# Performance work log

Measured on AMD Instinct MI355X. Metric: run time of the kernel, lower is better.

## Reference

```python
import jax, jax.numpy as jnp
import numpy as np

B, S, D, H = 2, 2048, 1024, 16
EPS = 1e-7  # keras backend epsilon

def setup_inputs() -> dict:
    key = jax.random.key(0)
    ks = jax.random.split(key, 5)
    x = jax.random.normal(ks[0], (B, S, D), dtype=jnp.float32)
    # mem_mask convention: attend where mem_mask == 0 (causal here)
    i = jnp.arange(S)
    causal = (i[None, :] > i[:, None]).astype(jnp.float32)  # 1 = masked
    mem_mask = jnp.broadcast_to(causal[None, None], (B, 1, S, S))
    Wqkv = jax.random.normal(ks[1], (D, 3 * D), dtype=jnp.float32) * (D ** -0.5)
    W_out = jax.random.normal(ks[2], (D, D), dtype=jnp.float32) * (D ** -0.5)
    b_out = jnp.zeros((D,), dtype=jnp.float32)
    scale = jnp.ones((D,), dtype=jnp.float32)
    gate = jax.random.normal(ks[3], (D,), dtype=jnp.float32) * 0.02
    return {"x": x, "mem_mask": mem_mask, "Wqkv": Wqkv, "W_out": W_out,
            "b_out": b_out, "scale": scale, "gate": gate}

def reference(x, mem_mask, Wqkv, W_out, b_out, scale, gate):
    b, s, d = x.shape
    dh = d // H
    h = jnp.einsum('bsd,de->bse', x, Wqkv)
    q, k, v = jnp.split(h, 3, axis=-1)
    def split_heads(t):
        return t.reshape(b, s, H, dh).transpose(0, 2, 1, 3)  # [B,H,S,dh]
    q, k, v = split_heads(q), split_heads(k), split_heads(v)
    q = q * (dh ** -0.5)
    logits = jnp.einsum('bhqd,bhkd->bhqk', q, k)
    logits = logits * (mem_mask == 0.0).astype(logits.dtype)
    weights = jax.nn.relu(logits)
    o = jnp.einsum('bhqk,bhkd->bhqd', weights, v)
    o = o.transpose(0, 2, 1, 3).reshape(b, s, d)  # combine heads
    # Gated RMSNorm
    ms = jnp.mean(o * o, axis=-1, keepdims=True)
    o = scale * o * jax.lax.rsqrt(ms + EPS) * jax.nn.sigmoid(gate * o)
    return jnp.einsum('bsd,de->bse', o, W_out) + b_out
```

## Files before the change

### kernel.cpp

```cpp
#include <hip/hip_runtime.h>
#include <hip/hip_bf16.h>

typedef unsigned short u16;
typedef __attribute__((ext_vector_type(8))) short bf16x8;
typedef __attribute__((ext_vector_type(4))) short short4v;
typedef __attribute__((ext_vector_type(4))) float floatx4;
typedef __attribute__((ext_vector_type(2))) unsigned uint2v;

__device__ __forceinline__ float bf2f(u16 u) {
    unsigned v = ((unsigned)u) << 16;
    return __builtin_bit_cast(float, v);
}
__device__ __forceinline__ u16 f2bf(float f) {
    unsigned u = __builtin_bit_cast(unsigned, f);
    u += 0x7fffu + ((u >> 16) & 1u);
    return (u16)(u >> 16);
}

#define GLDS16(g, l)                                                             \
    __builtin_amdgcn_global_load_lds(                                            \
        (const __attribute__((address_space(1))) void*)(g),                      \
        (__attribute__((address_space(3))) void*)(l), 16, 0, 0)

__global__ __launch_bounds__(256) void cvt_bf16(const float* __restrict__ in, u16* __restrict__ out) {
    const int i = blockIdx.x * 256 + threadIdx.x;
    const floatx4 v = ((const floatx4*)in)[i];
    short4v o;
#pragma unroll
    for (int j = 0; j < 4; ++j) o[j] = (short)f2bf(v[j]);
    ((short4v*)out)[i] = o;
}

__global__ void wtrans(const float* __restrict__ in, u16* __restrict__ out, int R, int C) {
    __shared__ u16 t[32][33];
    const int c0 = blockIdx.x * 32, r0 = blockIdx.y * 32;
    const int x = threadIdx.x, y = threadIdx.y;
#pragma unroll
    for (int i = 0; i < 32; i += 8) t[y + i][x] = f2bf(in[(size_t)(r0 + y + i) * C + c0 + x]);
    __syncthreads();
#pragma unroll
    for (int i = 0; i < 32; i += 8) out[(size_t)(c0 + y + i) * R + r0 + x] = t[x][y + i];
}

__global__ void vtrans(const u16* __restrict__ h, u16* __restrict__ vt) {
    __shared__ u16 t[32][33];
    const int bh = blockIdx.z;
    const int b = bh >> 4, hd = bh & 15;
    const int s0 = blockIdx.x * 32, d0 = blockIdx.y * 32;
    const int x = threadIdx.x, y = threadIdx.y;
    const u16* in = h + (size_t)(b * 2048) * 3072 + 2048 + hd * 64;
#pragma unroll
    for (int i = 0; i < 32; i += 8) t[y + i][x] = in[(size_t)(s0 + y + i) * 3072 + d0 + x];
    __syncthreads();
    u16* o = vt + (size_t)bh * 64 * 2048;
#pragma unroll
    for (int i = 0; i < 32; i += 8) {
        const float f = bf2f(t[x][y + i]) * 0.125f;
        o[(size_t)(d0 + y + i) * 2048 + s0 + x] = (u16)(__builtin_bit_cast(unsigned, f) >> 16);
    }
}

template <int TM, bool BIAS, typename OUT>
__global__ __launch_bounds__(256) void gemm_bt(const u16* __restrict__ A, const u16* __restrict__ Bt,
                                               OUT* __restrict__ C, const float* __restrict__ bias,
                                               int M, int N, int K) {
    constexpr int MI = TM / 32;
    __shared__ u16 sA[TM * 32];
    __shared__ u16 sB[128 * 32];
    const int tid = threadIdx.x;
    const int lane = tid & 63, wave = tid >> 6;
    const int l15 = lane & 15, quad = lane >> 4;
    const int row0 = blockIdx.y * TM, col0 = blockIdx.x * 128;
    const int wm = (wave & 1) * (TM / 2), wn = (wave >> 1) * 64;
    const int c_ = (tid & 3) << 3;
    floatx4 acc[MI][4] = {};
    for (int k0 = 0; k0 < K; k0 += 32) {
#pragma unroll
        for (int it = 0; it < 2; ++it) {
            const int idx = it * 256 + tid;
            const int r = idx >> 2;
            GLDS16(Bt + (size_t)(col0 + r) * K + k0 + c_, sB + idx * 8);
        }
#pragma unroll
        for (int it = 0; it < TM / 64; ++it) {
            const int idx = it * 256 + tid;
            const int r = idx >> 2;
            GLDS16(A + (size_t)(row0 + r) * K + k0 + c_, sA + idx * 8);
        }
        __syncthreads();
        bf16x8 af[MI], bfr[4];
#pragma unroll
        for (int i = 0; i < MI; ++i) af[i] = *(const bf16x8*)(sA + (wm + i * 16 + l15) * 32 + quad * 8);
#pragma unroll
        for (int j = 0; j < 4; ++j) bfr[j] = *(const bf16x8*)(sB + (wn + j * 16 + l15) * 32 + quad * 8);
#pragma unroll
        for (int i = 0; i < MI; ++i)
#pragma unroll
            for (int j = 0; j < 4; ++j)
                acc[i][j] = __builtin_amdgcn_mfma_f32_16x16x32_bf16(af[i], bfr[j], acc[i][j], 0, 0, 0);
        __syncthreads();
    }
#pragma unroll
    for (int i = 0; i < MI; ++i) {
#pragma unroll
        for (int j = 0; j < 4; ++j) {
            const int col = col0 + wn + j * 16 + l15;
            const int row = row0 + wm + i * 16 + quad * 4;
            const float b = BIAS ? bias[col] : 0.f;
#pragma unroll
            for (int r = 0; r < 4; ++r) {
                const float v = acc[i][j][r] + b;
                if constexpr (sizeof(OUT) == 2)
                    C[(size_t)(row + r) * N + col] = (OUT)f2bf(v);
                else
                    C[(size_t)(row + r) * N + col] = (OUT)v;
            }
        }
    }
}

__device__ __forceinline__ void pack_store(floatx4 s, u16* dst, bool diag, int kgb, int qg) {
    float v0 = fmaxf(s[0], 0.f), v1 = fmaxf(s[1], 0.f);
    float v2 = fmaxf(s[2], 0.f), v3 = fmaxf(s[3], 0.f);
    if (diag) {
        if (kgb + 0 > qg) v0 = 0.f;
        if (kgb + 1 > qg) v1 = 0.f;
        if (kgb + 2 > qg) v2 = 0.f;
        if (kgb + 3 > qg) v3 = 0.f;
    }
    uint2v p;
    p.x = ((__builtin_bit_cast(unsigned, v0) + 0x8000u) >> 16) |
          ((__builtin_bit_cast(unsigned, v1) + 0x8000u) & 0xffff0000u);
    p.y = ((__builtin_bit_cast(unsigned, v2) + 0x8000u) >> 16) |
          ((__builtin_bit_cast(unsigned, v3) + 0x8000u) & 0xffff0000u);
    *(uint2v*)dst = p;
}

__global__ __launch_bounds__(256) void relu_attn(const u16* __restrict__ h, const u16* __restrict__ vt,
                                                 float* __restrict__ o) {
    __shared__ u16 sK[64 * 72];
    __shared__ u16 sV[64 * 72];
    __shared__ u16 sP[128 * 72];
    const int bid = blockIdx.x;
    const int pr = bid >> 5;
    const int bh = bid & 31;
    const int b = bh >> 4, hd = bh & 15;
    const int qtl = pr, qth = 31 - pr;
    const int tid = threadIdx.x, lane = tid & 63, wave = tid >> 6;
    const int l15 = lane & 15, quad = lane >> 4;

    bf16x8 qfl[2], qfh[2];
    {
        const u16* ql = h + (size_t)(b * 2048 + qtl * 64 + wave * 16 + l15) * 3072 + hd * 64;
        const u16* qh = h + (size_t)(b * 2048 + qth * 64 + wave * 16 + l15) * 3072 + hd * 64;
#pragma unroll
        for (int ks = 0; ks < 2; ++ks) {
            qfl[ks] = *(const bf16x8*)(ql + ks * 32 + quad * 8);
            qfh[ks] = *(const bf16x8*)(qh + ks * 32 + quad * 8);
        }
    }

    floatx4 accl[4] = {}, acch[4] = {};
    const u16* kbase = h + (size_t)(b * 2048) * 3072 + 1024 + hd * 64;
    const u16* vbase = vt + (size_t)bh * 64 * 2048;
    const int sr = tid >> 3;
    const int sc = (tid & 7) << 3;
    const int qg = wave * 16 + l15;

    for (int kc = 0; kc <= qth; ++kc) {
        const int c0 = kc * 64;
#pragma unroll
        for (int it = 0; it < 2; ++it) {
            const int r = it * 32 + sr;
            bf16x8 kv = *(const bf16x8*)(kbase + (size_t)(c0 + r) * 3072 + sc);
            bf16x8 vv = *(const bf16x8*)(vbase + (size_t)r * 2048 + c0 + sc);
            *(bf16x8*)(sK + r * 72 + sc) = kv;
            *(bf16x8*)(sV + r * 72 + sc) = vv;
        }
        __syncthreads();
        const bool lact = (kc <= qtl);
        const floatx4 z = {0.f, 0.f, 0.f, 0.f};
#pragma unroll
        for (int mt = 0; mt < 4; ++mt) {
            const bf16x8 kf0 = *(const bf16x8*)(sK + (mt * 16 + l15) * 72 + quad * 8);
            const bf16x8 kf1 = *(const bf16x8*)(sK + (mt * 16 + l15) * 72 + 32 + quad * 8);
            const int kgb = mt * 16 + quad * 4;
            floatx4 s = __builtin_amdgcn_mfma_f32_16x16x32_bf16(kf0, qfh[0], z, 0, 0, 0);
            s = __builtin_amdgcn_mfma_f32_16x16x32_bf16(kf1, qfh[1], s, 0, 0, 0);
            pack_store(s, sP + (size_t)(64 + qg) * 72 + kgb, kc == qth, kgb, qg);
            if (lact) {
                floatx4 t = __builtin_amdgcn_mfma_f32_16x16x32_bf16(kf0, qfl[0], z, 0, 0, 0);
                t = __builtin_amdgcn_mfma_f32_16x16x32_bf16(kf1, qfl[1], t, 0, 0, 0);
                pack_store(t, sP + (size_t)qg * 72 + kgb, kc == qtl, kgb, qg);
            }
        }
#pragma unroll
        for (int kb = 0; kb < 2; ++kb) {
            const bf16x8 pfh = *(const bf16x8*)(sP + (size_t)(64 + wave * 16 + l15) * 72 + kb * 32 + quad * 8);
#pragma unroll
            for (int nt = 0; nt < 4; ++nt) {
                const bf16x8 vf = *(const bf16x8*)(sV + (nt * 16 + l15) * 72 + kb * 32 + quad * 8);
                acch[nt] = __builtin_amdgcn_mfma_f32_16x16x32_bf16(pfh, vf, acch[nt], 0, 0, 0);
                if (lact) {
                    const bf16x8 pfl = *(const bf16x8*)(sP + (size_t)(wave * 16 + l15) * 72 + kb * 32 + quad * 8);
                    accl[nt] = __builtin_amdgcn_mfma_f32_16x16x32_bf16(pfl, vf, accl[nt], 0, 0, 0);
                }
            }
        }
        __syncthreads();
    }
#pragma unroll
    for (int nt = 0; nt < 4; ++nt) {
        const int col = hd * 64 + nt * 16 + l15;
        const int rl = qtl * 64 + wave * 16 + quad * 4;
        const int rh = qth * 64 + wave * 16 + quad * 4;
#pragma unroll
        for (int r = 0; r < 4; ++r) {
            o[(size_t)(b * 2048 + rl + r) * 1024 + col] = accl[nt][r];
            o[(size_t)(b * 2048 + rh + r) * 1024 + col] = acch[nt][r];
        }
    }
}

__global__ __launch_bounds__(256) void rms_gate(const float* __restrict__ o, const float* __restrict__ scale,
                                                const float* __restrict__ gate, u16* __restrict__ out) {
    const int row = blockIdx.x;
    const int tid = threadIdx.x;
    const floatx4* op = (const floatx4*)(o + (size_t)row * 1024);
    floatx4 v = op[tid];
    float ss = v[0] * v[0] + v[1] * v[1] + v[2] * v[2] + v[3] * v[3];
#pragma unroll
    for (int m = 32; m >= 1; m >>= 1) ss += __shfl_xor(ss, m, 64);
    __shared__ float red[4];
    if ((tid & 63) == 0) red[tid >> 6] = ss;
    __syncthreads();
    const float ms = (red[0] + red[1] + red[2] + red[3]) * (1.0f / 1024.0f);
    const float inv = rsqrtf(ms + 1e-7f);
    const int c = tid * 4;
#pragma unroll
    for (int j = 0; j < 4; ++j) {
        const float s = scale[c + j];
        const float g = gate[c + j];
        const float x = v[j];
        const float sig = 1.0f / (1.0f + __expf(-g * x));
        out[(size_t)row * 1024 + c + j] = f2bf(s * x * inv * sig);
    }
}

extern "C" void kernel_launch(void* const* d_in, const int* in_sizes, int n_in,
                              void* d_out, int out_size, void* d_ws, size_t ws_size,
                              hipStream_t stream) {
    const float* x     = (const float*)d_in[0];
    const float* Wqkv  = (const float*)d_in[2];
    const float* Wout  = (const float*)d_in[3];
    const float* bout  = (const float*)d_in[4];
    const float* scale = (const float*)d_in[5];
    const float* gate  = (const float*)d_in[6];
    float* out = (float*)d_out;

    char* p = (char*)d_ws;
    u16* xb    = (u16*)p; p += (size_t)4096 * 1024 * 2;
    u16* h     = (u16*)p; p += (size_t)4096 * 3072 * 2;
    u16* vt    = (u16*)p; p += (size_t)32 * 64 * 2048 * 2;
    u16* WqkvT = (u16*)p; p += (size_t)3072 * 1024 * 2;
    u16* WoutT = (u16*)p; p += (size_t)1024 * 1024 * 2;
    float* oat = (float*)p; p += (size_t)4096 * 1024 * 4;
    u16* onorm = (u16*)p; p += (size_t)4096 * 1024 * 2;

    cvt_bf16<<<4096, 256, 0, stream>>>(x, xb);
    wtrans<<<dim3(96, 32), dim3(32, 8), 0, stream>>>(Wqkv, WqkvT, 1024, 3072);
    wtrans<<<dim3(32, 32), dim3(32, 8), 0, stream>>>(Wout, WoutT, 1024, 1024);
    gemm_bt<128, false, u16><<<dim3(24, 32), 256, 0, stream>>>(xb, WqkvT, h, nullptr, 4096, 3072, 1024);
    vtrans<<<dim3(64, 2, 32), dim3(32, 8), 0, stream>>>(h, vt);
    relu_attn<<<512, 256, 0, stream>>>(h, vt, oat);
    rms_gate<<<4096, 256, 0, stream>>>(oat, scale, gate, onorm);
    gemm_bt<64, true, float><<<dim3(8, 64), 256, 0, stream>>>(onorm, WoutT, out, bout, 4096, 1024, 1024);
}
```

Baseline: 225.4 us.

## Split causal attention over key ranges with atomic accumulation for more blocks

Replaces the paired low/high query-tile scheme with a split-K style decomposition. Each block processes one query tile over a range of at most eight key chunks, launching 2560 blocks instead of 512. Partial outputs are accumulated with float atomicAdd into a buffer that the conversion kernel now zeroes. This aims to fix low occupancy and load imbalance, at the cost of atomic traffic, an extra zeroing write, and nondeterministic summation order.

```diff
diff --git a/kernel.cpp b/kernel.cpp
--- a/kernel.cpp
+++ b/kernel.cpp
@@ -22,13 +22,16 @@
         (const __attribute__((address_space(1))) void*)(g),                      \
         (__attribute__((address_space(3))) void*)(l), 16, 0, 0)
 
-__global__ __launch_bounds__(256) void cvt_bf16(const float* __restrict__ in, u16* __restrict__ out) {
+__global__ __launch_bounds__(256) void cvt_bf16(const float* __restrict__ in, u16* __restrict__ out,
+                                                float* __restrict__ oz) {
     const int i = blockIdx.x * 256 + threadIdx.x;
     const floatx4 v = ((const floatx4*)in)[i];
     short4v o;
 #pragma unroll
     for (int j = 0; j < 4; ++j) o[j] = (short)f2bf(v[j]);
     ((short4v*)out)[i] = o;
+    const floatx4 z = {0.f, 0.f, 0.f, 0.f};
+    ((floatx4*)oz)[i] = z;
 }
 
 __global__ void wtrans(const float* __restrict__ in, u16* __restrict__ out, int R, int C) {
@@ -140,34 +143,33 @@
                                                  float* __restrict__ o) {
     __shared__ u16 sK[64 * 72];
     __shared__ u16 sV[64 * 72];
-    __shared__ u16 sP[128 * 72];
+    __shared__ u16 sP[64 * 72];
     const int bid = blockIdx.x;
-    const int pr = bid >> 5;
     const int bh = bid & 31;
+    const int p = bid >> 5;
+    int s, qt;
+    if (p < 32)      { s = 0; qt = 31 - p; }
+    else if (p < 56) { s = 1; qt = 31 - (p - 32); }
+    else if (p < 72) { s = 2; qt = 31 - (p - 56); }
+    else             { s = 3; qt = 31 - (p - 72); }
     const int b = bh >> 4, hd = bh & 15;
-    const int qtl = pr, qth = 31 - pr;
     const int tid = threadIdx.x, lane = tid & 63, wave = tid >> 6;
     const int l15 = lane & 15, quad = lane >> 4;
-
-    bf16x8 qfl[2], qfh[2];
-    {
-        const u16* ql = h + (size_t)(b * 2048 + qtl * 64 + wave * 16 + l15) * 3072 + hd * 64;
-        const u16* qh = h + (size_t)(b * 2048 + qth * 64 + wave * 16 + l15) * 3072 + hd * 64;
-#pragma unroll
-        for (int ks = 0; ks < 2; ++ks) {
-            qfl[ks] = *(const bf16x8*)(ql + ks * 32 + quad * 8);
-            qfh[ks] = *(const bf16x8*)(qh + ks * 32 + quad * 8);
-        }
-    }
-
-    floatx4 accl[4] = {}, acch[4] = {};
+    const int q0 = qt * 64;
+    const int c_lo = s * 8, c_hi = min(s * 8 + 7, qt);
+
+    const u16* qrow = h + (size_t)(b * 2048 + q0 + wave * 16 + l15) * 3072 + hd * 64;
+    bf16x8 qf0 = *(const bf16x8*)(qrow + quad * 8);
+    bf16x8 qf1 = *(const bf16x8*)(qrow + 32 + quad * 8);
+
+    floatx4 acc[4] = {};
     const u16* kbase = h + (size_t)(b * 2048) * 3072 + 1024 + hd * 64;
     const u16* vbase = vt + (size_t)bh * 64 * 2048;
     const int sr = tid >> 3;
     const int sc = (tid & 7) << 3;
     const int qg = wave * 16 + l15;
 
-    for (int kc = 0; kc <= qth; ++kc) {
+    for (int kc = c_lo; kc <= c_hi; ++kc) {
         const int c0 = kc * 64;
 #pragma unroll
         for (int it = 0; it < 2; ++it) {
@@ -178,33 +180,24 @@
             *(bf16x8*)(sV + r * 72 + sc) = vv;
         }
         __syncthreads();
-        const bool lact = (kc <= qtl);
+        const bool diag = (kc == qt);
         const floatx4 z = {0.f, 0.f, 0.f, 0.f};
 #pragma unroll
         for (int mt = 0; mt < 4; ++mt) {
             const bf16x8 kf0 = *(const bf16x8*)(sK + (mt * 16 + l15) * 72 + quad * 8);
             const bf16x8 kf1 = *(const bf16x8*)(sK + (mt * 16 + l15) * 72 + 32 + quad * 8);
             const int kgb = mt * 16 + quad * 4;
-            floatx4 s = __builtin_amdgcn_mfma_f32_16x16x32_bf16(kf0, qfh[0], z, 0, 0, 0);
-            s = __builtin_amdgcn_mfma_f32_16x16x32_bf16(kf1, qfh[1], s, 0, 0, 0);
-            pack_store(s, sP + (size_t)(64 + qg) * 72 + kgb, kc == qth, kgb, qg);
-            if (lact) {
-                floatx4 t = __builtin_amdgcn_mfma_f32_16x16x32_bf16(kf0, qfl[0], z, 0, 0, 0);
-                t = __builtin_amdgcn_mfma_f32_16x16x32_bf16(kf1, qfl[1], t, 0, 0, 0);
-                pack_store(t, sP + (size_t)qg * 72 + kgb, kc == qtl, kgb, qg);
-            }
+            floatx4 sv_ = __builtin_amdgcn_mfma_f32_16x16x32_bf16(kf0, qf0, z, 0, 0, 0);
+            sv_ = __builtin_amdgcn_mfma_f32_16x16x32_bf16(kf1, qf1, sv_, 0, 0, 0);
+            pack_store(sv_, sP + (size_t)qg * 72 + kgb, diag, kgb, qg);
         }
 #pragma unroll
         for (int kb = 0; kb < 2; ++kb) {
-            const bf16x8 pfh = *(const bf16x8*)(sP + (size_t)(64 + wave * 16 + l15) * 72 + kb * 32 + quad * 8);
+            const bf16x8 pf = *(const bf16x8*)(sP + (size_t)(wave * 16 + l15) * 72 + kb * 32 + quad * 8);
 #pragma unroll
             for (int nt = 0; nt < 4; ++nt) {
                 const bf16x8 vf = *(const bf16x8*)(sV + (nt * 16 + l15) * 72 + kb * 32 + quad * 8);
-                acch[nt] = __builtin_amdgcn_mfma_f32_16x16x32_bf16(pfh, vf, acch[nt], 0, 0, 0);
-                if (lact) {
-                    const bf16x8 pfl = *(const bf16x8*)(sP + (size_t)(wave * 16 + l15) * 72 + kb * 32 + quad * 8);
-                    accl[nt] = __builtin_amdgcn_mfma_f32_16x16x32_bf16(pfl, vf, accl[nt], 0, 0, 0);
-                }
+                acc[nt] = __builtin_amdgcn_mfma_f32_16x16x32_bf16(pf, vf, acc[nt], 0, 0, 0);
             }
         }
         __syncthreads();
@@ -212,13 +205,10 @@
 #pragma unroll
     for (int nt = 0; nt < 4; ++nt) {
         const int col = hd * 64 + nt * 16 + l15;
-        const int rl = qtl * 64 + wave * 16 + quad * 4;
-        const int rh = qth * 64 + wave * 16 + quad * 4;
-#pragma unroll
-        for (int r = 0; r < 4; ++r) {
-            o[(size_t)(b * 2048 + rl + r) * 1024 + col] = accl[nt][r];
-            o[(size_t)(b * 2048 + rh + r) * 1024 + col] = acch[nt][r];
-        }
+        const int row = q0 + wave * 16 + quad * 4;
+#pragma unroll
+        for (int r = 0; r < 4; ++r)
+            atomicAdd(&o[(size_t)(b * 2048 + row + r) * 1024 + col], acc[nt][r]);
     }
 }
 
@@ -267,12 +257,12 @@
     float* oat = (float*)p; p += (size_t)4096 * 1024 * 4;
     u16* onorm = (u16*)p; p += (size_t)4096 * 1024 * 2;
 
-    cvt_bf16<<<4096, 256, 0, stream>>>(x, xb);
+    cvt_bf16<<<4096, 256, 0, stream>>>(x, xb, oat);
     wtrans<<<dim3(96, 32), dim3(32, 8), 0, stream>>>(Wqkv, WqkvT, 1024, 3072);
     wtrans<<<dim3(32, 32), dim3(32, 8), 0, stream>>>(Wout, WoutT, 1024, 1024);
     gemm_bt<128, false, u16><<<dim3(24, 32), 256, 0, stream>>>(xb, WqkvT, h, nullptr, 4096, 3072, 1024);
     vtrans<<<dim3(64, 2, 32), dim3(32, 8), 0, stream>>>(h, vt);
-    relu_attn<<<512, 256, 0, stream>>>(h, vt, oat);
+    relu_attn<<<2560, 256, 0, stream>>>(h, vt, oat);
     rms_gate<<<4096, 256, 0, stream>>>(oat, scale, gate, onorm);
     gemm_bt<64, true, float><<<dim3(8, 64), 256, 0, stream>>>(onorm, WoutT, out, bout, 4096, 1024, 1024);
 }
```

New measurement: 230.0 us. +2.0%, slower.

## Merge prep kernels and fuse V transpose into QKV GEMM epilogue

Applied to the files above, without the earlier changes.

Combines the x conversion and both weight transposes into a single launch, and drops the separate vtrans kernel by having the QKV GEMM epilogue write the scaled, transposed V tile directly. This removes three launches and an extra read and write pass over V. In exchange the GEMM epilogue does more stores (4-element strided writes for V columns), and vt rounding now uses round-to-nearest instead of truncation.

```diff
diff --git a/kernel.cpp b/kernel.cpp
--- a/kernel.cpp
+++ b/kernel.cpp
@@ -22,48 +22,36 @@
         (const __attribute__((address_space(1))) void*)(g),                      \
         (__attribute__((address_space(3))) void*)(l), 16, 0, 0)
 
-__global__ __launch_bounds__(256) void cvt_bf16(const float* __restrict__ in, u16* __restrict__ out) {
-    const int i = blockIdx.x * 256 + threadIdx.x;
-    const floatx4 v = ((const floatx4*)in)[i];
-    short4v o;
-#pragma unroll
-    for (int j = 0; j < 4; ++j) o[j] = (short)f2bf(v[j]);
-    ((short4v*)out)[i] = o;
-}
-
-__global__ void wtrans(const float* __restrict__ in, u16* __restrict__ out, int R, int C) {
+__global__ __launch_bounds__(256) void prep(const float* __restrict__ x, u16* __restrict__ xb,
+                                            const float* __restrict__ Wqkv, u16* __restrict__ WqkvT,
+                                            const float* __restrict__ Wout, u16* __restrict__ WoutT) {
     __shared__ u16 t[32][33];
-    const int c0 = blockIdx.x * 32, r0 = blockIdx.y * 32;
-    const int x = threadIdx.x, y = threadIdx.y;
-#pragma unroll
-    for (int i = 0; i < 32; i += 8) t[y + i][x] = f2bf(in[(size_t)(r0 + y + i) * C + c0 + x]);
+    int blk = blockIdx.x;
+    if (blk < 4096) {
+        const int i = blk * 256 + threadIdx.x;
+        const floatx4 v = ((const floatx4*)x)[i];
+        short4v o;
+#pragma unroll
+        for (int j = 0; j < 4; ++j) o[j] = (short)f2bf(v[j]);
+        ((short4v*)xb)[i] = o;
+        return;
+    }
+    const float* in; u16* out; int R, C, bx, by;
+    if (blk < 4096 + 3072) { blk -= 4096; in = Wqkv; out = WqkvT; R = 1024; C = 3072; bx = blk % 96; by = blk / 96; }
+    else                   { blk -= 7168; in = Wout; out = WoutT; R = 1024; C = 1024; bx = blk & 31; by = blk >> 5; }
+    const int c0 = bx * 32, r0 = by * 32;
+    const int xx = threadIdx.x & 31, yy = threadIdx.x >> 5;
+#pragma unroll
+    for (int i = 0; i < 32; i += 8) t[yy + i][xx] = f2bf(in[(size_t)(r0 + yy + i) * C + c0 + xx]);
     __syncthreads();
 #pragma unroll
-    for (int i = 0; i < 32; i += 8) out[(size_t)(c0 + y + i) * R + r0 + x] = t[x][y + i];
-}
-
-__global__ void vtrans(const u16* __restrict__ h, u16* __restrict__ vt) {
-    __shared__ u16 t[32][33];
-    const int bh = blockIdx.z;
-    const int b = bh >> 4, hd = bh & 15;
-    const int s0 = blockIdx.x * 32, d0 = blockIdx.y * 32;
-    const int x = threadIdx.x, y = threadIdx.y;
-    const u16* in = h + (size_t)(b * 2048) * 3072 + 2048 + hd * 64;
-#pragma unroll
-    for (int i = 0; i < 32; i += 8) t[y + i][x] = in[(size_t)(s0 + y + i) * 3072 + d0 + x];
-    __syncthreads();
-    u16* o = vt + (size_t)bh * 64 * 2048;
-#pragma unroll
-    for (int i = 0; i < 32; i += 8) {
-        const float f = bf2f(t[x][y + i]) * 0.125f;
-        o[(size_t)(d0 + y + i) * 2048 + s0 + x] = (u16)(__builtin_bit_cast(unsigned, f) >> 16);
-    }
-}
-
-template <int TM, bool BIAS, typename OUT>
+    for (int i = 0; i < 32; i += 8) out[(size_t)(c0 + yy + i) * R + r0 + xx] = t[xx][yy + i];
+}
+
+template <int TM, bool BIAS, typename OUT, bool VT>
 __global__ __launch_bounds__(256) void gemm_bt(const u16* __restrict__ A, const u16* __restrict__ Bt,
                                                OUT* __restrict__ C, const float* __restrict__ bias,
-                                               int M, int N, int K) {
+                                               u16* __restrict__ vtp, int M, int N, int K) {
     constexpr int MI = TM / 32;
     __shared__ u16 sA[TM * 32];
     __shared__ u16 sB[128 * 32];
@@ -107,6 +95,7 @@
             const int col = col0 + wn + j * 16 + l15;
             const int row = row0 + wm + i * 16 + quad * 4;
             const float b = BIAS ? bias[col] : 0.f;
+            short4v pk;
 #pragma unroll
             for (int r = 0; r < 4; ++r) {
                 const float v = acc[i][j][r] + b;
@@ -114,6 +103,14 @@
                     C[(size_t)(row + r) * N + col] = (OUT)f2bf(v);
                 else
                     C[(size_t)(row + r) * N + col] = (OUT)v;
+                if constexpr (VT) pk[r] = (short)f2bf(v * 0.125f);
+            }
+            if constexpr (VT) {
+                if (col0 >= 2048) {
+                    const int bb = row >> 11, s = row & 2047;
+                    const int hd = (col - 2048) >> 6, dh = col & 63;
+                    *(short4v*)(vtp + ((size_t)(bb * 16 + hd) * 64 + dh) * 2048 + s) = pk;
+                }
             }
         }
     }
@@ -267,12 +264,9 @@
     float* oat = (float*)p; p += (size_t)4096 * 1024 * 4;
     u16* onorm = (u16*)p; p += (size_t)4096 * 1024 * 2;
 
-    cvt_bf16<<<4096, 256, 0, stream>>>(x, xb);
-    wtrans<<<dim3(96, 32), dim3(32, 8), 0, stream>>>(Wqkv, WqkvT, 1024, 3072);
-    wtrans<<<dim3(32, 32), dim3(32, 8), 0, stream>>>(Wout, WoutT, 1024, 1024);
-    gemm_bt<128, false, u16><<<dim3(24, 32), 256, 0, stream>>>(xb, WqkvT, h, nullptr, 4096, 3072, 1024);
-    vtrans<<<dim3(64, 2, 32), dim3(32, 8), 0, stream>>>(h, vt);
+    prep<<<8192, 256, 0, stream>>>(x, xb, Wqkv, WqkvT, Wout, WoutT);
+    gemm_bt<128, false, u16, true><<<dim3(24, 32), 256, 0, stream>>>(xb, WqkvT, h, nullptr, vt, 4096, 3072, 1024);
     relu_attn<<<512, 256, 0, stream>>>(h, vt, oat);
     rms_gate<<<4096, 256, 0, stream>>>(oat, scale, gate, onorm);
-    gemm_bt<64, true, float><<<dim3(8, 64), 256, 0, stream>>>(onorm, WoutT, out, bout, 4096, 1024, 1024);
-}
+    gemm_bt<64, true, float, false><<<dim3(8, 64), 256, 0, stream>>>(onorm, WoutT, out, bout, nullptr, 4096, 1024, 1024);
+}
```

Result: faster. 218.7 us (-3.0%).
